# Kernel optimization log

Hardware: AMD Instinct MI355X
Metric: run time of the kernel (lower is better)

Reference implementation:

```python
import jax, jax.numpy as jnp
import numpy as np
from jax import lax

EPS = 1e-08
PAD = 1  # kernel_size // 2 for k=3


def setup_inputs() -> dict:
    key = jax.random.key(0)
    k1, k2, k3, k4 = jax.random.split(key, 4)
    B, Cin, Cout, H, W, K, S = 16, 256, 256, 64, 64, 3, 512
    x = jax.random.normal(k1, (B, Cin, H, W), dtype=jnp.float32)
    style = jax.random.normal(k2, (B, S), dtype=jnp.float32)
    mod_weight = jax.random.normal(k3, (Cin, S), dtype=jnp.float32)
    mod_bias = jnp.zeros((Cin,), dtype=jnp.float32)
    weight = jax.random.normal(k4, (1, Cout, Cin, K, K), dtype=jnp.float32)
    bias = jnp.zeros((1, Cout, 1, 1), dtype=jnp.float32)
    return {"x": x, "style": style, "mod_weight": mod_weight,
            "mod_bias": mod_bias, "weight": weight, "bias": bias}


def reference(x, style, mod_weight, mod_bias, weight, bias):
    # EqualizedLinear modulation (lr_mul = 1.0): s[b, cin]
    s = style @ mod_weight.T + mod_bias  # [B, Cin]
    # per-sample modulated weights: [B, Cout, Cin, K, K]
    w = weight * s[:, None, :, None, None]
    # demodulation: rsqrt of sum over (Cin, K, K)
    demod = lax.rsqrt(jnp.sum(w * w, axis=(2, 3, 4)) + EPS)  # [B, Cout]
    w = w * demod[:, :, None, None, None]

    # per-sample conv2d (groups=B equivalent) via vmap over batch
    def conv_one(xb, wb):
        # xb: [Cin, H, W], wb: [Cout, Cin, K, K]
        return lax.conv_general_dilated(
            xb[None], wb, window_strides=(1, 1),
            padding=[(PAD, PAD), (PAD, PAD)],
            dimension_numbers=("NCHW", "OIHW", "NCHW"))[0]

    out = jax.vmap(conv_one)(x, w)  # [B, Cout, H, W]
    return out + bias
```

## Files before the change

kernel.cpp:

```cpp
#include <hip/hip_runtime.h>

#define EPS 1e-8f
#define THREADS 512

typedef __attribute__((ext_vector_type(8))) short short8;
typedef __attribute__((ext_vector_type(4))) float f32x4;
typedef __attribute__((ext_vector_type(8))) unsigned short u16x8;

static __device__ __forceinline__ unsigned short f2bf(float f) {
  unsigned int u = __float_as_uint(f);
  u += 0x7FFF + ((u >> 16) & 1);
  return (unsigned short)(u >> 16);
}

__global__ void k_style(const float* __restrict__ style, const float* __restrict__ mw,
                        const float* __restrict__ mb, float* __restrict__ s_out) {
  int b = blockIdx.x, t = threadIdx.x;
  __shared__ float st[512];
  st[t]       = style[b*512 + t];
  st[t + 256] = style[b*512 + 256 + t];
  __syncthreads();
  const float4* row = (const float4*)(mw + (size_t)t*512);
  float acc = 0.f;
#pragma unroll 4
  for (int i = 0; i < 128; ++i) {
    float4 m = row[i];
    acc += m.x*st[4*i] + m.y*st[4*i+1] + m.z*st[4*i+2] + m.w*st[4*i+3];
  }
  s_out[b*256 + t] = acc + mb[t];
}

__global__ void k_wprep(const float* __restrict__ weight, float* __restrict__ wsq,
                        unsigned short* __restrict__ wbf) {
  int idx = blockIdx.x*256 + threadIdx.x;
  int co = idx >> 8, ci = idx & 255;
  const float* wp = weight + (size_t)idx*9;
  int c = ci >> 6, cil = ci & 63;
  int base = ((co*128 + cil*2) ^ ((co & 7) << 4)) >> 1;
  float sum = 0.f;
#pragma unroll
  for (int r = 0; r < 9; ++r) {
    float v = wp[r];
    sum += v*v;
    wbf[(size_t)(c*9 + r)*16384 + base] = f2bf(v);
  }
  wsq[idx] = sum;
}

__global__ void k_demod(const float* __restrict__ s, const float* __restrict__ wsq,
                        float* __restrict__ dm) {
  int b = blockIdx.x, t = threadIdx.x;
  __shared__ float s2[256];
  float sv = s[b*256 + t];
  s2[t] = sv*sv;
  __syncthreads();
  const float4* row = (const float4*)(wsq + (size_t)t*256);
  float acc = 0.f;
#pragma unroll 4
  for (int i = 0; i < 64; ++i) {
    float4 q = row[i];
    acc += q.x*s2[4*i] + q.y*s2[4*i+1] + q.z*s2[4*i+2] + q.w*s2[4*i+3];
  }
  dm[b*256 + t] = rsqrtf(acc + EPS);
}

__global__ void k_pad(const float* __restrict__ x, const float* __restrict__ s,
                      unsigned short* __restrict__ xp) {
  int bid = blockIdx.x;
  int b = bid / 66, gh = bid - b*66;
  int t = threadIdx.x;
  size_t rowbase = (size_t)(b*66 + gh) * (66*256);
  u16x8* rp = (u16x8*)(xp + rowbase);
  if (gh == 0 || gh == 65) {
    u16x8 z = (u16x8)0;
    for (int q = t; q < 2112; q += 256) rp[q] = z;
    return;
  }
  int h = gh - 1;
  __shared__ float sl[256];
  __shared__ unsigned short xl[64*256];
  sl[t] = s[b*256 + t];
  __syncthreads();
  int w = t & 63, cq = t >> 6;
#pragma unroll 4
  for (int c0 = 0; c0 < 256; c0 += 4) {
    int ci = c0 + cq;
    float v = x[((size_t)(b*256 + ci)*64 + h)*64 + w] * sl[ci];
    int byte = w*512 + (((ci >> 3) ^ (w & 31)) << 4) + (ci & 7)*2;
    xl[byte >> 1] = f2bf(v);
  }
  __syncthreads();
  u16x8 z = (u16x8)0;
  if (t < 32) rp[t] = z;
  else if (t < 64) rp[65*32 + (t - 32)] = z;
  for (int q = t; q < 2048; q += 256) {
    int w2 = q >> 5, slot = q & 31;
    u16x8 v = *(const u16x8*)&xl[(w2*512 + ((slot ^ (w2 & 31)) << 4)) >> 1];
    rp[(w2 + 1)*32 + slot] = v;
  }
}

__global__ __launch_bounds__(512, 2)
void k_conv(const unsigned short* __restrict__ xp, const unsigned short* __restrict__ wbf,
            const float* __restrict__ dm, const float* __restrict__ bias,
            float* __restrict__ out) {
  __shared__ unsigned short x_lds[6*66*64];
  __shared__ unsigned short w_lds[256*64];

  const int tid = threadIdx.x;
  const int lane = tid & 63;
  const int wave = tid >> 6;
  const int b = blockIdx.x >> 4;
  const int h0 = (blockIdx.x & 15) * 4;
  const int wm = wave >> 1, wn = wave & 1;
  const int l15 = lane & 15, lk = lane >> 4;

  f32x4 acc[4][8];
#pragma unroll
  for (int m = 0; m < 4; ++m)
#pragma unroll
    for (int f = 0; f < 8; ++f) acc[m][f] = (f32x4)0.f;

  for (int c = 0; c < 4; ++c) {
    __syncthreads();
    {
      int cb = c*64;
      for (int it = 0; it < 7; ++it) {
        int q = it*THREADS + tid;
        if (q < 3168) {
          int hw = q >> 3;
          int hl = hw / 66, w = hw - hl*66;
          int slot = (q & 7) ^ (hw & 7);
          const unsigned short* src =
              xp + (size_t)((b*66 + h0 + hl)*66 + w)*256 + cb + slot*8;
          __builtin_amdgcn_global_load_lds(
              (const __attribute__((address_space(1))) void*)src,
              (__attribute__((address_space(3))) void*)&x_lds[(size_t)q*8],
              16, 0, 0);
        }
      }
    }
    for (int r = 0; r < 9; ++r) {
      if (r) __syncthreads();
      {
        const unsigned short* wsrc = wbf + (size_t)(c*9 + r)*16384;
#pragma unroll
        for (int it = 0; it < 4; ++it) {
          int q = it*THREADS + tid;
          __builtin_amdgcn_global_load_lds(
              (const __attribute__((address_space(1))) void*)(wsrc + (size_t)q*8),
              (__attribute__((address_space(3))) void*)&w_lds[(size_t)q*8],
              16, 0, 0);
        }
      }
      __syncthreads();
      int dh = r / 3, dw = r - dh*3;
#pragma unroll
      for (int kh = 0; kh < 2; ++kh) {
        int cio = (kh*32 + lk*8)*2;
        short8 a[4], bf[8];
#pragma unroll
        for (int m = 0; m < 4; ++m) {
          int co = wm*64 + m*16 + l15;
          int byte = (co*128 + cio) ^ ((co & 7) << 4);
          a[m] = *(const short8*)((const char*)w_lds + byte);
        }
#pragma unroll
        for (int f = 0; f < 8; ++f) {
          int row = (wn*2 + (f >> 2) + dh)*66 + ((f & 3)*16 + l15 + dw);
          int byte = (row*128 + cio) ^ ((row & 7) << 4);
          bf[f] = *(const short8*)((const char*)x_lds + byte);
        }
#pragma unroll
        for (int m = 0; m < 4; ++m)
#pragma unroll
          for (int f = 0; f < 8; ++f)
            acc[m][f] = __builtin_amdgcn_mfma_f32_16x16x32_bf16(a[m], bf[f], acc[m][f], 0, 0, 0);
      }
    }
  }

  int colane = (lane >> 4) * 4;
#pragma unroll
  for (int m = 0; m < 4; ++m) {
    int cob = wm*64 + m*16 + colane;
    float4 d4 = *(const float4*)&dm[b*256 + cob];
    float4 b4 = *(const float4*)&bias[cob];
#pragma unroll
    for (int f = 0; f < 8; ++f) {
      int h = h0 + wn*2 + (f >> 2);
      int wc = (f & 3)*16 + l15;
      float* op = out + ((size_t)(b*256 + cob)*64 + h)*64 + wc;
      op[0]     = acc[m][f][0] * d4.x + b4.x;
      op[4096]  = acc[m][f][1] * d4.y + b4.y;
      op[8192]  = acc[m][f][2] * d4.z + b4.z;
      op[12288] = acc[m][f][3] * d4.w + b4.w;
    }
  }
}

extern "C" void kernel_launch(void* const* d_in, const int* in_sizes, int n_in,
                              void* d_out, int out_size, void* d_ws, size_t ws_size,
                              hipStream_t stream) {
  const float* x      = (const float*)d_in[0];
  const float* style  = (const float*)d_in[1];
  const float* mw     = (const float*)d_in[2];
  const float* mb     = (const float*)d_in[3];
  const float* weight = (const float*)d_in[4];
  const float* bias   = (const float*)d_in[5];
  float* out = (float*)d_out;

  char* ws = (char*)d_ws;
  float* s_buf        = (float*)(ws);
  float* wsq          = (float*)(ws + 16384);
  float* dmod         = (float*)(ws + 16384 + 262144);
  unsigned short* wbf = (unsigned short*)(ws + 294912);
  unsigned short* xpd = (unsigned short*)(ws + 294912 + 1179648);

  k_style<<<16, 256, 0, stream>>>(style, mw, mb, s_buf);
  k_wprep<<<256, 256, 0, stream>>>(weight, wsq, wbf);
  k_demod<<<16, 256, 0, stream>>>(s_buf, wsq, dmod);
  k_pad<<<16*66, 256, 0, stream>>>(x, s_buf, xpd);
  k_conv<<<256, 512, 0, stream>>>(xpd, wbf, dmod, bias, out);
}
```

Measured before the change: 231.0 us.

## Halve conv tile height, fuse prep kernels, vectorize pad loads

The conv kernel now computes 2 output rows per block instead of 4, which doubles the grid to 512 blocks and cuts the accumulators to 4x4. It raises the launch bound to 4 blocks per CU and remaps block indices across batches. The style and weight-prep kernels are merged into one launch, and weight reads are staged through shared memory for coalescing. The pad kernel reads float4 along width and writes 8-channel vectors into LDS. Smaller tiles mean less weight reuse per x tile, so weight LDS traffic per output doubles, in exchange for higher occupancy and better load balance.

```diff
diff --git a/kernel.cpp b/kernel.cpp
--- a/kernel.cpp
+++ b/kernel.cpp
@@ -13,38 +13,42 @@
   return (unsigned short)(u >> 16);
 }
 
-__global__ void k_style(const float* __restrict__ style, const float* __restrict__ mw,
-                        const float* __restrict__ mb, float* __restrict__ s_out) {
-  int b = blockIdx.x, t = threadIdx.x;
-  __shared__ float st[512];
-  st[t]       = style[b*512 + t];
-  st[t + 256] = style[b*512 + 256 + t];
-  __syncthreads();
-  const float4* row = (const float4*)(mw + (size_t)t*512);
-  float acc = 0.f;
+__global__ void k_prep(const float* __restrict__ style, const float* __restrict__ mw,
+                       const float* __restrict__ mb, float* __restrict__ s_out,
+                       const float* __restrict__ weight, float* __restrict__ wsq,
+                       unsigned short* __restrict__ wbf) {
+  __shared__ float sm[2304];
+  int t = threadIdx.x;
+  if (blockIdx.x < 16) {
+    int b = blockIdx.x;
+    sm[t]       = style[b*512 + t];
+    sm[t + 256] = style[b*512 + 256 + t];
+    __syncthreads();
+    const float4* row = (const float4*)(mw + (size_t)t*512);
+    float acc = 0.f;
 #pragma unroll 4
-  for (int i = 0; i < 128; ++i) {
-    float4 m = row[i];
-    acc += m.x*st[4*i] + m.y*st[4*i+1] + m.z*st[4*i+2] + m.w*st[4*i+3];
-  }
-  s_out[b*256 + t] = acc + mb[t];
-}
-
-__global__ void k_wprep(const float* __restrict__ weight, float* __restrict__ wsq,
-                        unsigned short* __restrict__ wbf) {
-  int idx = blockIdx.x*256 + threadIdx.x;
-  int co = idx >> 8, ci = idx & 255;
-  const float* wp = weight + (size_t)idx*9;
-  int c = ci >> 6, cil = ci & 63;
-  int base = ((co*128 + cil*2) ^ ((co & 7) << 4)) >> 1;
-  float sum = 0.f;
-#pragma unroll
-  for (int r = 0; r < 9; ++r) {
-    float v = wp[r];
-    sum += v*v;
-    wbf[(size_t)(c*9 + r)*16384 + base] = f2bf(v);
-  }
-  wsq[idx] = sum;
+    for (int i = 0; i < 128; ++i) {
+      float4 m = row[i];
+      acc += m.x*sm[4*i] + m.y*sm[4*i+1] + m.z*sm[4*i+2] + m.w*sm[4*i+3];
+    }
+    s_out[b*256 + t] = acc + mb[t];
+  } else {
+    int co = blockIdx.x - 16;
+    for (int q = t; q < 576; q += 256)
+      *(float4*)&sm[q*4] = *(const float4*)(weight + (size_t)co*2304 + q*4);
+    __syncthreads();
+    int ci = t;
+    int c = ci >> 6, cil = ci & 63;
+    int base = ((co*128 + cil*2) ^ ((co & 7) << 4)) >> 1;
+    float sum = 0.f;
+#pragma unroll
+    for (int r = 0; r < 9; ++r) {
+      float v = sm[ci*9 + r];
+      sum += v*v;
+      wbf[(size_t)(c*9 + r)*16384 + base] = f2bf(v);
+    }
+    wsq[co*256 + ci] = sum;
+  }
 }
 
 __global__ void k_demod(const float* __restrict__ s, const float* __restrict__ wsq,
@@ -81,13 +85,27 @@
   __shared__ unsigned short xl[64*256];
   sl[t] = s[b*256 + t];
   __syncthreads();
-  int w = t & 63, cq = t >> 6;
-#pragma unroll 4
-  for (int c0 = 0; c0 < 256; c0 += 4) {
-    int ci = c0 + cq;
-    float v = x[((size_t)(b*256 + ci)*64 + h)*64 + w] * sl[ci];
-    int byte = w*512 + (((ci >> 3) ^ (w & 31)) << 4) + (ci & 7)*2;
-    xl[byte >> 1] = f2bf(v);
+  int w4 = (t & 15) * 4, o0 = t >> 4;
+#pragma unroll
+  for (int p = 0; p < 2; ++p) {
+    int oct = o0 + p*16;
+    u16x8 outv[4];
+#pragma unroll
+    for (int j = 0; j < 8; ++j) {
+      int ci = oct*8 + j;
+      float4 v = *(const float4*)(x + ((size_t)(b*256 + ci)*64 + h)*64 + w4);
+      float sc = sl[ci];
+      outv[0][j] = (short)f2bf(v.x * sc);
+      outv[1][j] = (short)f2bf(v.y * sc);
+      outv[2][j] = (short)f2bf(v.z * sc);
+      outv[3][j] = (short)f2bf(v.w * sc);
+    }
+#pragma unroll
+    for (int k = 0; k < 4; ++k) {
+      int w = w4 + k;
+      int byte = w*512 + ((oct ^ (w & 31)) << 4);
+      *(u16x8*)((char*)xl + byte) = outv[k];
+    }
   }
   __syncthreads();
   u16x8 z = (u16x8)0;
@@ -95,39 +113,41 @@
   else if (t < 64) rp[65*32 + (t - 32)] = z;
   for (int q = t; q < 2048; q += 256) {
     int w2 = q >> 5, slot = q & 31;
-    u16x8 v = *(const u16x8*)&xl[(w2*512 + ((slot ^ (w2 & 31)) << 4)) >> 1];
+    u16x8 v = *(const u16x8*)((char*)xl + w2*512 + ((slot ^ (w2 & 31)) << 4));
     rp[(w2 + 1)*32 + slot] = v;
   }
 }
 
-__global__ __launch_bounds__(512, 2)
+__global__ __launch_bounds__(512, 4)
 void k_conv(const unsigned short* __restrict__ xp, const unsigned short* __restrict__ wbf,
             const float* __restrict__ dm, const float* __restrict__ bias,
             float* __restrict__ out) {
-  __shared__ unsigned short x_lds[6*66*64];
+  __shared__ unsigned short x_lds[4*66*64];
   __shared__ unsigned short w_lds[256*64];
 
   const int tid = threadIdx.x;
   const int lane = tid & 63;
   const int wave = tid >> 6;
-  const int b = blockIdx.x >> 4;
-  const int h0 = (blockIdx.x & 15) * 4;
+  const int bid = (blockIdx.x & 7)*64 + (blockIdx.x >> 3);
+  const int b = bid >> 5;
+  const int h0 = (bid & 31) * 2;
   const int wm = wave >> 1, wn = wave & 1;
   const int l15 = lane & 15, lk = lane >> 4;
 
-  f32x4 acc[4][8];
+  f32x4 acc[4][4];
 #pragma unroll
   for (int m = 0; m < 4; ++m)
 #pragma unroll
-    for (int f = 0; f < 8; ++f) acc[m][f] = (f32x4)0.f;
+    for (int f = 0; f < 4; ++f) acc[m][f] = (f32x4)0.f;
 
   for (int c = 0; c < 4; ++c) {
     __syncthreads();
     {
       int cb = c*64;
-      for (int it = 0; it < 7; ++it) {
+#pragma unroll
+      for (int it = 0; it < 5; ++it) {
         int q = it*THREADS + tid;
-        if (q < 3168) {
+        if (q < 2112) {
           int hw = q >> 3;
           int hl = hw / 66, w = hw - hl*66;
           int slot = (q & 7) ^ (hw & 7);
@@ -158,7 +178,7 @@
 #pragma unroll
       for (int kh = 0; kh < 2; ++kh) {
         int cio = (kh*32 + lk*8)*2;
-        short8 a[4], bf[8];
+        short8 a[4], bf[4];
 #pragma unroll
         for (int m = 0; m < 4; ++m) {
           int co = wm*64 + m*16 + l15;
@@ -166,15 +186,15 @@
           a[m] = *(const short8*)((const char*)w_lds + byte);
         }
 #pragma unroll
-        for (int f = 0; f < 8; ++f) {
-          int row = (wn*2 + (f >> 2) + dh)*66 + ((f & 3)*16 + l15 + dw);
+        for (int f = 0; f < 4; ++f) {
+          int row = (wn + dh)*66 + (f*16 + l15 + dw);
           int byte = (row*128 + cio) ^ ((row & 7) << 4);
           bf[f] = *(const short8*)((const char*)x_lds + byte);
         }
 #pragma unroll
         for (int m = 0; m < 4; ++m)
 #pragma unroll
-          for (int f = 0; f < 8; ++f)
+          for (int f = 0; f < 4; ++f)
             acc[m][f] = __builtin_amdgcn_mfma_f32_16x16x32_bf16(a[m], bf[f], acc[m][f], 0, 0, 0);
       }
     }
@@ -186,10 +206,10 @@
     int cob = wm*64 + m*16 + colane;
     float4 d4 = *(const float4*)&dm[b*256 + cob];
     float4 b4 = *(const float4*)&bias[cob];
-#pragma unroll
-    for (int f = 0; f < 8; ++f) {
-      int h = h0 + wn*2 + (f >> 2);
-      int wc = (f & 3)*16 + l15;
+    int h = h0 + wn;
+#pragma unroll
+    for (int f = 0; f < 4; ++f) {
+      int wc = f*16 + l15;
       float* op = out + ((size_t)(b*256 + cob)*64 + h)*64 + wc;
       op[0]     = acc[m][f][0] * d4.x + b4.x;
       op[4096]  = acc[m][f][1] * d4.y + b4.y;
@@ -217,9 +237,8 @@
   unsigned short* wbf = (unsigned short*)(ws + 294912);
   unsigned short* xpd = (unsigned short*)(ws + 294912 + 1179648);
 
-  k_style<<<16, 256, 0, stream>>>(style, mw, mb, s_buf);
-  k_wprep<<<256, 256, 0, stream>>>(weight, wsq, wbf);
+  k_prep<<<272, 256, 0, stream>>>(style, mw, mb, s_buf, weight, wsq, wbf);
   k_demod<<<16, 256, 0, stream>>>(s_buf, wsq, dmod);
   k_pad<<<16*66, 256, 0, stream>>>(x, s_buf, xpd);
-  k_conv<<<256, 512, 0, stream>>>(xpd, wbf, dmod, bias, out);
-}
+  k_conv<<<512, 512, 0, stream>>>(xpd, wbf, dmod, bias, out);
+}
```

Result: slower. 248.6 us (+7.6%).
